# Optimization experiments

Measured on AMD Instinct MI355X. Metric: run time of the kernel, lower is better.

## Reference

```python
import jax, jax.numpy as jnp
from jax import lax
import numpy as np

HEADS = 4
BUCKET = 64
DEPTH = 4


def _conv(x, w, b):
    y = lax.conv_general_dilated(x, w, (1, 1), [(1, 1), (1, 1)],
                                 dimension_numbers=('NCHW', 'OIHW', 'NCHW'))
    return y + b[None, :, None, None]


def _convT(x, w, b):
    # torch ConvTranspose2d(k=4, s=2, p=1): flip kernel, swap io, lhs_dilation=2, pad k-1-p=2
    wk = jnp.flip(w, (2, 3)).transpose(1, 0, 2, 3)
    y = lax.conv_general_dilated(x, wk, (1, 1), [(2, 2), (2, 2)], lhs_dilation=(2, 2),
                                 dimension_numbers=('NCHW', 'OIHW', 'NCHW'))
    return y + b[None, :, None, None]


def _maxpool(x):
    return lax.reduce_window(x, -jnp.inf, lax.max, (1, 1, 2, 2), (1, 1, 2, 2), 'VALID')


def _ln(x, g, b):
    m = x.mean(-1, keepdims=True)
    v = ((x - m) ** 2).mean(-1, keepdims=True)
    return (x - m) / jnp.sqrt(v + 1e-5) * g + b


def _lsh_attention(x, Wqk, bqk, Wv, bv, Wo, bo, rot):
    # shared-QK LSH bucketed attention (single hash round), look-one-back chunks
    B, N, D = x.shape
    h, dh = HEADS, D // HEADS
    qk = (x @ Wqk + bqk).reshape(B, N, h, dh).transpose(0, 2, 1, 3)  # B h N dh
    v = (x @ Wv + bv).reshape(B, N, h, dh).transpose(0, 2, 1, 3)
    k = qk / (jnp.linalg.norm(qk, axis=-1, keepdims=True) + 1e-6)    # keys = normalized queries
    rotated = jnp.einsum('bhnd,hdr->bhnr', qk, rot)
    buckets = jnp.argmax(jnp.concatenate([rotated, -rotated], -1), -1)  # B h N
    ticker = jnp.arange(N)
    perm = jnp.argsort(buckets * N + ticker, axis=-1)  # stable sort by bucket
    inv_perm = jnp.argsort(perm, axis=-1)
    g = lambda t: jnp.take_along_axis(t, perm[..., None], axis=2)
    nc = N // BUCKET
    bq = g(qk).reshape(B, h, nc, BUCKET, dh)
    bk = g(k).reshape(B, h, nc, BUCKET, dh)
    bv_ = g(v).reshape(B, h, nc, BUCKET, dh)
    bk2 = jnp.concatenate([bk, jnp.roll(bk, 1, axis=2)], axis=3)   # look one chunk back
    bv2 = jnp.concatenate([bv_, jnp.roll(bv_, 1, axis=2)], axis=3)
    dots = jnp.einsum('bhcid,bhcjd->bhcij', bq, bk2) * (dh ** -0.5)
    spos = jnp.take_along_axis(jnp.broadcast_to(ticker, buckets.shape), perm, -1).reshape(B, h, nc, BUCKET)
    kpos = jnp.concatenate([spos, jnp.roll(spos, 1, axis=2)], axis=3)
    dots = jnp.where(spos[..., :, None] == kpos[..., None, :], -1e5, dots)  # mask self (q == k)
    attn = jax.nn.softmax(dots, -1)
    o = jnp.einsum('bhcij,bhcjd->bhcid', attn, bv2).reshape(B, h, N, dh)
    o = jnp.take_along_axis(o, inv_perm[..., None], axis=2)  # unsort
    return o.transpose(0, 2, 1, 3).reshape(B, N, D) @ Wo + bo


def _reformer(seq, ln1_g, ln1_b, Wqk, bqk, Wv, bv, Wo, bo, rot, ln2_g, ln2_b, Wff1, bff1, Wff2, bff2):
    for i in range(DEPTH):
        seq = seq + _lsh_attention(_ln(seq, ln1_g[i], ln1_b[i]), Wqk[i], bqk[i], Wv[i], bv[i], Wo[i], bo[i], rot[i])
        hdn = jax.nn.gelu(_ln(seq, ln2_g[i], ln2_b[i]) @ Wff1[i] + bff1[i])
        seq = seq + hdn @ Wff2[i] + bff2[i]
    return seq


def _forward(burst, conv1_w, conv1_b, conv2_w, conv2_b, conv3_w, conv3_b,
             ln1_g, ln1_b, Wqk, bqk, Wv, bv, Wo, bo, rot, ln2_g, ln2_b,
             Wff1, bff1, Wff2, bff2, up1_w, up1_b, dec1_w, dec1_b,
             up2_w, up2_b, dec2_w, dec2_b, out_w, out_b):
    B, T, C, H, W = burst.shape
    x = burst.reshape(B * T, C, H, W)
    e1 = jax.nn.relu(_conv(x, conv1_w, conv1_b))
    p1 = _maxpool(e1)
    e2 = jax.nn.relu(_conv(p1, conv2_w, conv2_b))
    p2 = _maxpool(e2)
    bm = jax.nn.relu(_conv(p2, conv3_w, conv3_b))
    D = bm.shape[1]
    Hq, Wq = H // 4, W // 4
    seq = bm.transpose(0, 2, 3, 1).reshape(B * T, Hq * Wq, D)
    seq = _reformer(seq, ln1_g, ln1_b, Wqk, bqk, Wv, bv, Wo, bo, rot, ln2_g, ln2_b, Wff1, bff1, Wff2, bff2)
    bm = seq.reshape(B * T, Hq, Wq, D).transpose(0, 3, 1, 2)
    d1 = _convT(bm, up1_w, up1_b)
    d1 = jax.nn.relu(_conv(jnp.concatenate([d1, e2], 1), dec1_w, dec1_b))
    d2 = _convT(d1, up2_w, up2_b)
    d2 = jax.nn.relu(_conv(jnp.concatenate([d2, e1], 1), dec2_w, dec2_b))
    sharp = jax.nn.sigmoid(_conv(d2, out_w, out_b))
    return sharp.reshape(B, T, C, H, W)[:, 0]


def setup_inputs() -> dict:
    key = jax.random.key(0)
    ks = jax.random.split(key, 20)
    s = 0.05
    n = lambda k, shape: jax.random.normal(k, shape, jnp.float32) * s
    inp = {}
    inp['burst'] = jax.random.uniform(ks[0], (1, 7, 3, 256, 256), jnp.float32)
    inp['conv1_w'] = n(ks[1], (64, 3, 3, 3)); inp['conv1_b'] = jnp.zeros((64,), jnp.float32)
    inp['conv2_w'] = n(ks[2], (128, 64, 3, 3)); inp['conv2_b'] = jnp.zeros((128,), jnp.float32)
    inp['conv3_w'] = n(ks[3], (256, 128, 3, 3)); inp['conv3_b'] = jnp.zeros((256,), jnp.float32)
    inp['ln1_g'] = jnp.ones((4, 256), jnp.float32); inp['ln1_b'] = jnp.zeros((4, 256), jnp.float32)
    inp['Wqk'] = n(ks[4], (4, 256, 256)); inp['bqk'] = jnp.zeros((4, 256), jnp.float32)
    inp['Wv'] = n(ks[5], (4, 256, 256)); inp['bv'] = jnp.zeros((4, 256), jnp.float32)
    inp['Wo'] = n(ks[6], (4, 256, 256)); inp['bo'] = jnp.zeros((4, 256), jnp.float32)
    inp['rot'] = jax.random.normal(ks[7], (4, 4, 64, 32), jnp.float32)  # depth, heads, d_head, n_buckets//2
    inp['ln2_g'] = jnp.ones((4, 256), jnp.float32); inp['ln2_b'] = jnp.zeros((4, 256), jnp.float32)
    inp['Wff1'] = n(ks[8], (4, 256, 1024)); inp['bff1'] = jnp.zeros((4, 1024), jnp.float32)
    inp['Wff2'] = n(ks[9], (4, 1024, 256)); inp['bff2'] = jnp.zeros((4, 256), jnp.float32)
    inp['up1_w'] = n(ks[10], (256, 128, 4, 4)); inp['up1_b'] = jnp.zeros((128,), jnp.float32)
    inp['dec1_w'] = n(ks[11], (128, 256, 3, 3)); inp['dec1_b'] = jnp.zeros((128,), jnp.float32)
    inp['up2_w'] = n(ks[12], (128, 64, 4, 4)); inp['up2_b'] = jnp.zeros((64,), jnp.float32)
    inp['dec2_w'] = n(ks[13], (64, 128, 3, 3)); inp['dec2_b'] = jnp.zeros((64,), jnp.float32)
    inp['out_w'] = n(ks[14], (3, 64, 3, 3)); inp['out_b'] = jnp.zeros((3,), jnp.float32)
    return inp


def reference(burst, conv1_w, conv1_b, conv2_w, conv2_b, conv3_w, conv3_b,
              ln1_g, ln1_b, Wqk, bqk, Wv, bv, Wo, bo, rot, ln2_g, ln2_b,
              Wff1, bff1, Wff2, bff2, up1_w, up1_b, dec1_w, dec1_b,
              up2_w, up2_b, dec2_w, dec2_b, out_w, out_b):
    return _forward(burst, conv1_w, conv1_b, conv2_w, conv2_b, conv3_w, conv3_b,
                    ln1_g, ln1_b, Wqk, bqk, Wv, bv, Wo, bo, rot, ln2_g, ln2_b,
                    Wff1, bff1, Wff2, bff2, up1_w, up1_b, dec1_w, dec1_b,
                    up2_w, up2_b, dec2_w, dec2_b, out_w, out_b)
```

## Files before the change

kernel.cpp:

```cpp
#include <hip/hip_runtime.h>
#include <hip/hip_bf16.h>
#include <math.h>

using short8  = __attribute__((ext_vector_type(8))) short;
using half8   = __attribute__((ext_vector_type(8))) _Float16;
using floatx4 = __attribute__((ext_vector_type(4))) float;

static __device__ __forceinline__ float gelu_f(float x) {
    float x3 = x * x * x;
    return 0.5f * x * (1.f + tanhf(0.7978845608028654f * (x + 0.044715f * x3)));
}

static __device__ __forceinline__ short f2h(float f) {
    _Float16 h = (_Float16)f;
    return __builtin_bit_cast(short, h);
}


template <int OCB>
__global__ __launch_bounds__(256) void conv3x3_kernel(
    const float* __restrict__ in1, int C1, const float* __restrict__ in2, int C2,
    const float* __restrict__ w, const float* __restrict__ bias,
    float* __restrict__ out, int H, int W, int OC, int act, int nhwc_out)
{
    int tx = threadIdx.x, ty = threadIdx.y;
    int x = blockIdx.x * 16 + tx, y = blockIdx.y * 16 + ty;
    int oc0 = blockIdx.z * OCB;
    int C = C1 + C2;
    float acc[OCB];
#pragma unroll
    for (int o = 0; o < OCB; ++o) acc[o] = 0.f;
    for (int ic = 0; ic < C; ++ic) {
        const float* src = (ic < C1) ? (in1 + (size_t)ic * H * W)
                                     : (in2 + (size_t)(ic - C1) * H * W);
        float v[9];
#pragma unroll
        for (int ky = 0; ky < 3; ++ky) {
            int iy = y + ky - 1;
            bool okY = (iy >= 0) && (iy < H);
#pragma unroll
            for (int kx = 0; kx < 3; ++kx) {
                int ix = x + kx - 1;
                bool ok = okY && (ix >= 0) && (ix < W);
                v[ky * 3 + kx] = ok ? src[(size_t)iy * W + ix] : 0.f;
            }
        }
        const float* wp = w + ((size_t)oc0 * C + ic) * 9;
#pragma unroll
        for (int o = 0; o < OCB; ++o) {
            const float* wo = wp + (size_t)o * C * 9;
            acc[o] += v[0]*wo[0] + v[1]*wo[1] + v[2]*wo[2]
                    + v[3]*wo[3] + v[4]*wo[4] + v[5]*wo[5]
                    + v[6]*wo[6] + v[7]*wo[7] + v[8]*wo[8];
        }
    }
#pragma unroll
    for (int o = 0; o < OCB; ++o) {
        int oc = oc0 + o;
        float r = acc[o] + bias[oc];
        if (act == 1) r = fmaxf(r, 0.f);
        else if (act == 2) r = 1.f / (1.f + expf(-r));
        if (nhwc_out) out[(size_t)(y * W + x) * OC + oc] = r;
        else          out[(size_t)oc * H * W + (size_t)y * W + x] = r;
    }
}

__global__ __launch_bounds__(256) void conv3x3_lds_kernel(
    const float* __restrict__ in, const float* __restrict__ w,
    const float* __restrict__ bias, float* __restrict__ out,
    int H, int W, int C, int OC, int nhwc_out)
{
    __shared__ float s[16 * 324];
    int tid = threadIdx.x;
    int tx = tid & 15, ty = tid >> 4;
    int x0 = blockIdx.x * 16, y0 = blockIdx.y * 16;
    int oc0 = blockIdx.z * 8;
    int HW = H * W;
    float acc[8];
#pragma unroll
    for (int o = 0; o < 8; ++o) acc[o] = 0.f;
    for (int ic0 = 0; ic0 < C; ic0 += 16) {
        __syncthreads();
        for (int idx = tid; idx < 16 * 324; idx += 256) {
            int ic = idx / 324;
            int r = idx - ic * 324;
            int yy = r / 18;
            int xx = r - yy * 18;
            int gy = y0 + yy - 1, gx = x0 + xx - 1;
            float v = 0.f;
            if (gy >= 0 && gy < H && gx >= 0 && gx < W)
                v = in[(size_t)(ic0 + ic) * HW + (size_t)gy * W + gx];
            s[idx] = v;
        }
        __syncthreads();
        for (int ic = 0; ic < 16; ++ic) {
            const float* sc = s + ic * 324;
            float v[9];
            v[0] = sc[(ty + 0) * 18 + tx + 0];
            v[1] = sc[(ty + 0) * 18 + tx + 1];
            v[2] = sc[(ty + 0) * 18 + tx + 2];
            v[3] = sc[(ty + 1) * 18 + tx + 0];
            v[4] = sc[(ty + 1) * 18 + tx + 1];
            v[5] = sc[(ty + 1) * 18 + tx + 2];
            v[6] = sc[(ty + 2) * 18 + tx + 0];
            v[7] = sc[(ty + 2) * 18 + tx + 1];
            v[8] = sc[(ty + 2) * 18 + tx + 2];
            const float* wp = w + ((size_t)oc0 * C + ic0 + ic) * 9;
#pragma unroll
            for (int o = 0; o < 8; ++o) {
                const float* wo = wp + (size_t)o * C * 9;
                acc[o] += v[0]*wo[0] + v[1]*wo[1] + v[2]*wo[2]
                        + v[3]*wo[3] + v[4]*wo[4] + v[5]*wo[5]
                        + v[6]*wo[6] + v[7]*wo[7] + v[8]*wo[8];
            }
        }
    }
    int x = x0 + tx, y = y0 + ty;
#pragma unroll
    for (int o = 0; o < 8; ++o) {
        int oc = oc0 + o;
        float r = fmaxf(acc[o] + bias[oc], 0.f);
        if (nhwc_out) out[(size_t)(y * W + x) * OC + oc] = r;
        else          out[(size_t)oc * HW + (size_t)y * W + x] = r;
    }
}

__global__ __launch_bounds__(256) void maxpool_kernel(
    const float* __restrict__ in, float* __restrict__ out, int C, int IH, int IW)
{
    int OH = IH >> 1, OW = IW >> 1;
    int idx = blockIdx.x * 256 + threadIdx.x;
    int total = C * OH * OW;
    if (idx >= total) return;
    int x = idx % OW; int t = idx / OW; int y = t % OH; int c = t / OH;
    const float* p = in + (size_t)c * IH * IW + (size_t)(2 * y) * IW + 2 * x;
    out[idx] = fmaxf(fmaxf(p[0], p[1]), fmaxf(p[IW], p[IW + 1]));
}

__global__ __launch_bounds__(256) void ln_kernel(
    const float* __restrict__ x, const float* __restrict__ g,
    const float* __restrict__ b, float* __restrict__ y, short* __restrict__ yh)
{
    int wave = threadIdx.x >> 6, lane = threadIdx.x & 63;
    int n = blockIdx.x * 4 + wave;
    const float* xr = x + (size_t)n * 256;
    float4 v = *(const float4*)(xr + lane * 4);
    float s = v.x + v.y + v.z + v.w;
#pragma unroll
    for (int m = 1; m < 64; m <<= 1) s += __shfl_xor(s, m);
    float mean = s * (1.f / 256.f);
    float cx = v.x - mean, cy = v.y - mean, cz = v.z - mean, cw = v.w - mean;
    float q = cx * cx + cy * cy + cz * cz + cw * cw;
#pragma unroll
    for (int m = 1; m < 64; m <<= 1) q += __shfl_xor(q, m);
    float rstd = rsqrtf(q * (1.f / 256.f) + 1e-5f);
    float4 gv = *(const float4*)(g + lane * 4);
    float4 bv = *(const float4*)(b + lane * 4);
    float4 o;
    o.x = cx * rstd * gv.x + bv.x;
    o.y = cy * rstd * gv.y + bv.y;
    o.z = cz * rstd * gv.z + bv.z;
    o.w = cw * rstd * gv.w + bv.w;
    *(float4*)(y + (size_t)n * 256 + lane * 4) = o;
    short* yp = yh + (size_t)n * 256 + lane * 4;
    yp[0] = f2h(o.x); yp[1] = f2h(o.y); yp[2] = f2h(o.z); yp[3] = f2h(o.w);
}

static __device__ __forceinline__ void gemm_core(
    const float* __restrict__ A, const float* __restrict__ W,
    const float* __restrict__ bias, float* __restrict__ Cp,
    int N, int K, int act, int resid, int m0, int n0)
{
    __shared__ float As[16][68];
    __shared__ float Ws[16][68];
    int tid = threadIdx.x;
    int tx = tid & 15, ty = tid >> 4;
    int lm = tid & 63, lk = (tid >> 6) * 4;
    int lwk = tid >> 4, lwn = (tid & 15) * 4;
    const float* Ap = A + (size_t)(m0 + lm) * K + lk;
    const float* Wp = W + (size_t)lwk * N + n0 + lwn;
    float4 av = *(const float4*)Ap;
    float4 wv = *(const float4*)Wp;
    float acc[4][4];
#pragma unroll
    for (int i = 0; i < 4; ++i)
#pragma unroll
        for (int j = 0; j < 4; ++j) acc[i][j] = 0.f;
    for (int k0 = 0; k0 < K; k0 += 16) {
        As[lk + 0][lm] = av.x; As[lk + 1][lm] = av.y;
        As[lk + 2][lm] = av.z; As[lk + 3][lm] = av.w;
        *(float4*)(&Ws[lwk][lwn]) = wv;
        __syncthreads();
        if (k0 + 16 < K) {
            av = *(const float4*)(Ap + k0 + 16);
            wv = *(const float4*)(Wp + (size_t)(k0 + 16) * N);
        }
#pragma unroll
        for (int kk = 0; kk < 16; ++kk) {
            float4 a4 = *(const float4*)(&As[kk][ty * 4]);
            float4 w4 = *(const float4*)(&Ws[kk][tx * 4]);
            acc[0][0] += a4.x * w4.x; acc[0][1] += a4.x * w4.y; acc[0][2] += a4.x * w4.z; acc[0][3] += a4.x * w4.w;
            acc[1][0] += a4.y * w4.x; acc[1][1] += a4.y * w4.y; acc[1][2] += a4.y * w4.z; acc[1][3] += a4.y * w4.w;
            acc[2][0] += a4.z * w4.x; acc[2][1] += a4.z * w4.y; acc[2][2] += a4.z * w4.z; acc[2][3] += a4.z * w4.w;
            acc[3][0] += a4.w * w4.x; acc[3][1] += a4.w * w4.y; acc[3][2] += a4.w * w4.z; acc[3][3] += a4.w * w4.w;
        }
        __syncthreads();
    }
#pragma unroll
    for (int i = 0; i < 4; ++i) {
        int cm = m0 + ty * 4 + i;
#pragma unroll
        for (int j = 0; j < 4; ++j) {
            int cn = n0 + tx * 4 + j;
            float v = acc[i][j] + bias[cn];
            if (act == 1) v = gelu_f(v);
            float* cp = Cp + (size_t)cm * N + cn;
            if (resid) v += *cp;
            *cp = v;
        }
    }
}

__global__ __launch_bounds__(256) void gemm_kernel(
    const float* __restrict__ A, const float* __restrict__ W,
    const float* __restrict__ bias, float* __restrict__ C,
    int M, int N, int K, int act, int resid)
{
    gemm_core(A, W, bias, C, N, K, act, resid, blockIdx.y * 64, blockIdx.x * 64);
}

__global__ __launch_bounds__(256) void gemm_qkv_kernel(
    const float* __restrict__ A,
    const float* __restrict__ W1, const float* __restrict__ b1, float* __restrict__ C1,
    const float* __restrict__ W2, const float* __restrict__ b2, float* __restrict__ C2,
    int K)
{
    int side = blockIdx.x >> 2;
    const float* W = side ? W2 : W1;
    const float* b = side ? b2 : b1;
    float* C = side ? C2 : C1;
    gemm_core(A, W, b, C, 256, K, 0, 0, blockIdx.y * 64, (blockIdx.x & 3) * 64);
}

__global__ __launch_bounds__(256) void knorm_kernel(
    const float* __restrict__ qk, float* __restrict__ knrm)
{
    int t = blockIdx.x * 256 + threadIdx.x;
    int h = t >> 12, n = t & 4095;
    const float* q = qk + (size_t)n * 256 + h * 64;
    float s = 0.f;
#pragma unroll
    for (int d = 0; d < 64; d += 4) {
        float4 v = *(const float4*)(q + d);
        s += v.x * v.x + v.y * v.y + v.z * v.z + v.w * v.w;
    }
    knrm[t] = 1.f / (sqrtf(s) + 1e-6f);
}

__global__ __launch_bounds__(256) void bucket_kernel(
    const float* __restrict__ qk, const float* __restrict__ rot,
    int* __restrict__ buckets)
{
    int t = blockIdx.x * 256 + threadIdx.x;
    int h = t >> 12, n = t & 4095;
    const float* q = qk + (size_t)n * 256 + h * 64;
    const float* R = rot + (size_t)h * 2048;
    float acc[32];
#pragma unroll
    for (int r = 0; r < 32; ++r) acc[r] = 0.f;
    for (int d = 0; d < 64; ++d) {
        float qd = q[d];
        const float* Rd = R + d * 32;
#pragma unroll
        for (int r = 0; r < 32; ++r) acc[r] += qd * Rd[r];
    }
    float bvv = acc[0]; int best = 0;
#pragma unroll
    for (int j = 1; j < 64; ++j) {
        float val = (j < 32) ? acc[j] : -acc[j - 32];
        if (val > bvv) { bvv = val; best = j; }
    }
    buckets[t] = best;
}

__global__ __launch_bounds__(256) void lsh_sort_kernel(
    const int* __restrict__ buckets, int* __restrict__ perm)
{
    int h = blockIdx.x;
    const int* bk = buckets + h * 4096;
    __shared__ unsigned long long mask[64][64];
    __shared__ int counts[64];
    __shared__ int offsets[64];
    __shared__ int wpre[64][64];
    int tid = threadIdx.x, wave = tid >> 6, lane = tid & 63;
    for (int w = wave * 16; w < wave * 16 + 16; ++w) {
        int bl = bk[w * 64 + lane];
        for (int b = 0; b < 64; ++b) {
            unsigned long long m = __ballot(bl == b);
            if (lane == b) mask[b][w] = m;
        }
    }
    __syncthreads();
    if (tid < 64) {
        int c = 0;
        for (int w = 0; w < 64; ++w) c += __popcll(mask[tid][w]);
        counts[tid] = c;
    }
    __syncthreads();
    if (tid == 0) {
        int a = 0;
        for (int b = 0; b < 64; ++b) { offsets[b] = a; a += counts[b]; }
    }
    __syncthreads();
    for (int b = wave * 16; b < wave * 16 + 16; ++b) {
        int c = __popcll(mask[b][lane]);
        int incl = c;
#pragma unroll
        for (int off = 1; off < 64; off <<= 1) {
            int nb = __shfl_up(incl, off);
            if (lane >= off) incl += nb;
        }
        wpre[b][lane] = incl - c + offsets[b];
    }
    __syncthreads();
    for (int i = tid; i < 4096; i += 256) {
        int b = bk[i]; int w = i >> 6; int l = i & 63;
        unsigned long long below = mask[b][w] & ((1ull << l) - 1ull);
        int pos = wpre[b][w] + __popcll(below);
        perm[h * 4096 + pos] = i;
    }
}

__global__ __launch_bounds__(256) void attn_kernel(
    const float* __restrict__ qk, const float* __restrict__ vv,
    const float* __restrict__ knrm, const int* __restrict__ perm,
    float* __restrict__ o, short* __restrict__ oh)
{
    __shared__ float ks[128 * 64];
    __shared__ float dotsT[128 * 64];
    int c = blockIdx.x, h = blockIdx.y;
    int tid = threadIdx.x;
    const int* pm = perm + h * 4096;
    int cm = (c + 63) & 63;
    {
        int jr = tid >> 1, hf = tid & 1;
        int sk = (jr < 64) ? (c * 64 + jr) : (cm * 64 + (jr - 64));
        int nk = pm[sk];
        float sc = knrm[h * 4096 + nk];
        const float* src = qk + (size_t)nk * 256 + h * 64 + hf * 32;
        float* dst = ks + jr * 64 + hf * 32;
#pragma unroll
        for (int d = 0; d < 32; d += 4) {
            float4 v = *(const float4*)(src + d);
            v.x *= sc; v.y *= sc; v.z *= sc; v.w *= sc;
            *(float4*)(dst + d) = v;
        }
    }
    __syncthreads();
    int r = tid & 63, jg = tid >> 6;
    int nq = pm[c * 64 + r];
    {
        float qreg[64];
        const float* src = qk + (size_t)nq * 256 + h * 64;
#pragma unroll
        for (int d = 0; d < 64; d += 4) {
            float4 v = *(const float4*)(src + d);
            qreg[d] = v.x; qreg[d + 1] = v.y; qreg[d + 2] = v.z; qreg[d + 3] = v.w;
        }
        for (int j = jg * 32; j < jg * 32 + 32; ++j) {
            const float* kr = ks + j * 64;
            float dot = 0.f;
#pragma unroll
            for (int d = 0; d < 64; ++d) dot += qreg[d] * kr[d];
            int sk = (j < 64) ? (c * 64 + j) : (cm * 64 + (j - 64));
            int nk = pm[sk];
            dot = (nk == nq) ? -1e5f : dot * 0.125f;
            dotsT[j * 64 + r] = dot;
        }
    }
    __syncthreads();
    {
        int jr = tid >> 1, hf = tid & 1;
        int sk = (jr < 64) ? (c * 64 + jr) : (cm * 64 + (jr - 64));
        int nk = pm[sk];
        const float* src = vv + (size_t)nk * 256 + h * 64 + hf * 32;
        float* dst = ks + jr * 64 + hf * 32;
#pragma unroll
        for (int d = 0; d < 32; d += 4)
            *(float4*)(dst + d) = *(const float4*)(src + d);
    }
    if (tid < 64) {
        int rr = tid;
        float mx = -1e30f;
        for (int j = 0; j < 128; ++j) mx = fmaxf(mx, dotsT[j * 64 + rr]);
        float s = 0.f;
        for (int j = 0; j < 128; ++j) {
            float e = expf(dotsT[j * 64 + rr] - mx);
            dotsT[j * 64 + rr] = e; s += e;
        }
        float inv = 1.f / s;
        for (int j = 0; j < 128; ++j) dotsT[j * 64 + rr] *= inv;
    }
    __syncthreads();
    int dg = jg;
    float acc[16];
#pragma unroll
    for (int d = 0; d < 16; ++d) acc[d] = 0.f;
    for (int j = 0; j < 128; ++j) {
        float a = dotsT[j * 64 + r];
        const float* vr = ks + j * 64 + dg * 16;
#pragma unroll
        for (int d = 0; d < 16; ++d) acc[d] += a * vr[d];
    }
    size_t ob = (size_t)nq * 256 + h * 64 + dg * 16;
    float* dst = o + ob;
    short* dsth = oh + ob;
#pragma unroll
    for (int d = 0; d < 16; d += 4) {
        float4 v = { acc[d], acc[d + 1], acc[d + 2], acc[d + 3] };
        *(float4*)(dst + d) = v;
        dsth[d] = f2h(v.x); dsth[d+1] = f2h(v.y);
        dsth[d+2] = f2h(v.z); dsth[d+3] = f2h(v.w);
    }
}


__global__ void pack_gemm_kernel(const float* __restrict__ W, short* __restrict__ Bp,
                                 int N, int total)
{
    int t = blockIdx.x * 256 + threadIdx.x;
    if (t >= total) return;
    int lane = t & 63, fi = t >> 6;
    int NT = N >> 4;
    int nt = fi % NT, kt = fi / NT;
    int n = nt * 16 + (lane & 15);
    int k0 = kt * 32 + (lane >> 4) * 8;
    short8 v;
#pragma unroll
    for (int j = 0; j < 8; ++j) v[j] = f2h(W[(size_t)(k0 + j) * N + n]);
    ((short8*)Bp)[t] = v;
}

__global__ void pack_conv_kernel(const float* __restrict__ w, short* __restrict__ Bp,
                                 int C, int OC, int NT, int total)
{
    int t = blockIdx.x * 256 + threadIdx.x;
    if (t >= total) return;
    int lane = t & 63, fi = t >> 6;
    int nt = fi % NT, kt = fi / NT;
    int cpt = C >> 5;
    int tap = kt / cpt, ct = kt % cpt;
    int c = ct * 32 + (lane >> 4) * 8;
    int oc = nt * 16 + (lane & 15);
    short8 v;
#pragma unroll
    for (int j = 0; j < 8; ++j) {
        float f = (oc < OC) ? w[((size_t)oc * C + c + j) * 9 + tap] : 0.f;
        v[j] = f2h(f);
    }
    ((short8*)Bp)[t] = v;
}

__global__ void pack_convt_kernel(const float* __restrict__ w, short* __restrict__ Bp,
                                  int IC, int OC, int total)
{
    int t = blockIdx.x * 256 + threadIdx.x;
    if (t >= total) return;
    int lane = t & 63, fi = t >> 6;
    int NT = OC >> 4, cpt = IC >> 5, KT4 = 4 * cpt;
    int nt = fi % NT, r = fi / NT;
    int kt = r % KT4, pz = r / KT4;
    int py = pz >> 1, px = pz & 1;
    int t4 = kt / cpt, ct = kt % cpt;
    int ty = t4 >> 1, tx = t4 & 1;
    int ky = py ? (2 * ty) : (1 + 2 * ty);
    int kx = px ? (2 * tx) : (1 + 2 * tx);
    int ic = ct * 32 + (lane >> 4) * 8;
    int oc = nt * 16 + (lane & 15);
    short8 v;
#pragma unroll
    for (int j = 0; j < 8; ++j)
        v[j] = f2h(w[(((size_t)(ic + j) * OC + oc) * 4 + ky) * 4 + kx]);
    ((short8*)Bp)[t] = v;
}

__global__ __launch_bounds__(256) void gemm_mfma_kernel(
    const short* __restrict__ A, const short* __restrict__ Bp,
    const float* __restrict__ bias, float* __restrict__ Cf, short* __restrict__ Cb,
    int M, int N, int K, int act, int resid)
{
    int tid = threadIdx.x, wave = tid >> 6, lane = tid & 63;
    int quad = lane >> 4, l16 = lane & 15;
    int m0 = blockIdx.y * 64 + wave * 16;
    int NT = N >> 4;
    int nt0 = blockIdx.x * 4;
    const half8* arow = (const half8*)(A + (size_t)(m0 + l16) * K + quad * 8);
    const half8* bp = (const half8*)Bp;
    floatx4 acc0 = {0,0,0,0}, acc1 = {0,0,0,0}, acc2 = {0,0,0,0}, acc3 = {0,0,0,0};
    int KT = K >> 5;
    for (int kt = 0; kt < KT; ++kt) {
        half8 a = arow[kt * 4];
        size_t bi = ((size_t)kt * NT + nt0) * 64 + lane;
        acc0 = __builtin_amdgcn_mfma_f32_16x16x32_f16(a, bp[bi      ], acc0, 0, 0, 0);
        acc1 = __builtin_amdgcn_mfma_f32_16x16x32_f16(a, bp[bi +  64], acc1, 0, 0, 0);
        acc2 = __builtin_amdgcn_mfma_f32_16x16x32_f16(a, bp[bi + 128], acc2, 0, 0, 0);
        acc3 = __builtin_amdgcn_mfma_f32_16x16x32_f16(a, bp[bi + 192], acc3, 0, 0, 0);
    }
    floatx4 accs[4] = {acc0, acc1, acc2, acc3};
#pragma unroll
    for (int s = 0; s < 4; ++s) {
        int n = (nt0 + s) * 16 + l16;
        float bs = bias[n];
#pragma unroll
        for (int r = 0; r < 4; ++r) {
            int m = m0 + quad * 4 + r;
            float v = accs[s][r] + bs;
            if (act == 1) v = gelu_f(v);
            size_t o = (size_t)m * N + n;
            if (resid) v += Cf[o];
            if (Cb) Cb[o] = f2h(v);
            else    Cf[o] = v;
        }
    }
}

__global__ __launch_bounds__(256) void conv_mfma_kernel(
    const short* __restrict__ in1, int C1, const short* __restrict__ in2, int C2,
    const short* __restrict__ Bp, const float* __restrict__ bias,
    float* __restrict__ outf, short* __restrict__ outb, int H, int W, int OC)
{
    int tid = threadIdx.x, wave = tid >> 6, lane = tid & 63;
    int quad = lane >> 4, l16 = lane & 15;
    int x0 = blockIdx.x * 64, y = blockIdx.y, nt0 = blockIdx.z * 4;
    int C = C1 + C2, cpt = C >> 5, NT = OC >> 4;
    const half8* bp = (const half8*)Bp;
    floatx4 acc0 = {0,0,0,0}, acc1 = {0,0,0,0}, acc2 = {0,0,0,0}, acc3 = {0,0,0,0};
    int xm = x0 + wave * 16 + l16;
    for (int ky = 0; ky < 3; ++ky) {
        int yy = y + ky - 1;
        bool rok = (yy >= 0) && (yy < H);
        for (int kx = 0; kx < 3; ++kx) {
            int xx = xm + kx - 1;
            bool ok = rok && (xx >= 0) && (xx < W);
            int pos = yy * W + xx;
            int ktb = (ky * 3 + kx) * cpt;
            for (int ct = 0; ct < cpt; ++ct) {
                int cc = ct * 32 + quad * 8;
                half8 a = {};
                if (ok) {
                    const short* src = (cc < C1) ? (in1 + (size_t)pos * C1 + cc)
                                                 : (in2 + (size_t)pos * C2 + (cc - C1));
                    a = *(const half8*)src;
                }
                size_t bi = ((size_t)(ktb + ct) * NT + nt0) * 64 + lane;
                acc0 = __builtin_amdgcn_mfma_f32_16x16x32_f16(a, bp[bi      ], acc0, 0, 0, 0);
                acc1 = __builtin_amdgcn_mfma_f32_16x16x32_f16(a, bp[bi +  64], acc1, 0, 0, 0);
                acc2 = __builtin_amdgcn_mfma_f32_16x16x32_f16(a, bp[bi + 128], acc2, 0, 0, 0);
                acc3 = __builtin_amdgcn_mfma_f32_16x16x32_f16(a, bp[bi + 192], acc3, 0, 0, 0);
            }
        }
    }
    floatx4 accs[4] = {acc0, acc1, acc2, acc3};
#pragma unroll
    for (int s = 0; s < 4; ++s) {
        int n = (nt0 + s) * 16 + l16;
        float bs = bias[n];
#pragma unroll
        for (int r = 0; r < 4; ++r) {
            int m = wave * 16 + quad * 4 + r;
            int x = x0 + m;
            float v = fmaxf(accs[s][r] + bs, 0.f);
            size_t o = ((size_t)y * W + x) * OC + n;
            if (outb) outb[o] = f2h(v);
            else      outf[o] = v;
        }
    }
}

__global__ __launch_bounds__(256) void convt_mfma_kernel(
    const short* __restrict__ in, int IC, const short* __restrict__ Bp,
    const float* __restrict__ bias, short* __restrict__ outb, int IH, int IW, int OC)
{
    int tid = threadIdx.x, wave = tid >> 6, lane = tid & 63;
    int quad = lane >> 4, l16 = lane & 15;
    int pz = blockIdx.z & 3, nt0 = (blockIdx.z >> 2) * 4;
    int py = pz >> 1, px = pz & 1;
    int a0 = blockIdx.y, b0 = blockIdx.x * 64;
    int cpt = IC >> 5, NT = OC >> 4, KT4 = 4 * cpt;
    const half8* bp = (const half8*)Bp;
    floatx4 acc0 = {0,0,0,0}, acc1 = {0,0,0,0}, acc2 = {0,0,0,0}, acc3 = {0,0,0,0};
    int bm = b0 + wave * 16 + l16;
    for (int ty = 0; ty < 2; ++ty) {
        int iy = a0 + (py ? (1 - ty) : (-ty));
        bool rok = (iy >= 0) && (iy < IH);
        for (int tx = 0; tx < 2; ++tx) {
            int ix = bm + (px ? (1 - tx) : (-tx));
            bool ok = rok && (ix >= 0) && (ix < IW);
            int pos = iy * IW + ix;
            int ktb = (ty * 2 + tx) * cpt;
            for (int ct = 0; ct < cpt; ++ct) {
                int cc = ct * 32 + quad * 8;
                half8 a = {};
                if (ok) a = *(const half8*)(in + (size_t)pos * IC + cc);
                size_t bi = ((size_t)(pz * KT4 + ktb + ct) * NT + nt0) * 64 + lane;
                acc0 = __builtin_amdgcn_mfma_f32_16x16x32_f16(a, bp[bi      ], acc0, 0, 0, 0);
                acc1 = __builtin_amdgcn_mfma_f32_16x16x32_f16(a, bp[bi +  64], acc1, 0, 0, 0);
                acc2 = __builtin_amdgcn_mfma_f32_16x16x32_f16(a, bp[bi + 128], acc2, 0, 0, 0);
                acc3 = __builtin_amdgcn_mfma_f32_16x16x32_f16(a, bp[bi + 192], acc3, 0, 0, 0);
            }
        }
    }
    floatx4 accs[4] = {acc0, acc1, acc2, acc3};
    int OW = IW * 2;
    int oy = 2 * a0 + py;
#pragma unroll
    for (int s = 0; s < 4; ++s) {
        int n = (nt0 + s) * 16 + l16;
        float bs = bias[n];
#pragma unroll
        for (int r = 0; r < 4; ++r) {
            int m = wave * 16 + quad * 4 + r;
            int ox = 2 * (b0 + m) + px;
            float v = accs[s][r] + bs;
            outb[((size_t)oy * OW + ox) * OC + n] = f2h(v);
        }
    }
}

__global__ __launch_bounds__(256) void convout_mfma_kernel(
    const short* __restrict__ in, const short* __restrict__ Bp,
    const float* __restrict__ bias, float* __restrict__ out, int H, int W)
{
    int tid = threadIdx.x, wave = tid >> 6, lane = tid & 63;
    int quad = lane >> 4, l16 = lane & 15;
    int x0 = blockIdx.x * 64, y = blockIdx.y;
    const int C = 64, cpt = 2;
    const half8* bp = (const half8*)Bp;
    floatx4 acc = {0,0,0,0};
    int xm = x0 + wave * 16 + l16;
    for (int ky = 0; ky < 3; ++ky) {
        int yy = y + ky - 1;
        bool rok = (yy >= 0) && (yy < H);
        for (int kx = 0; kx < 3; ++kx) {
            int xx = xm + kx - 1;
            bool ok = rok && (xx >= 0) && (xx < W);
            int pos = yy * W + xx;
            int ktb = (ky * 3 + kx) * cpt;
#pragma unroll
            for (int ct = 0; ct < cpt; ++ct) {
                int cc = ct * 32 + quad * 8;
                half8 a = {};
                if (ok) a = *(const half8*)(in + (size_t)pos * C + cc);
                acc = __builtin_amdgcn_mfma_f32_16x16x32_f16(
                          a, bp[(size_t)(ktb + ct) * 64 + lane], acc, 0, 0, 0);
            }
        }
    }
    int oc = l16;
    if (oc < 3) {
        float bs = bias[oc];
#pragma unroll
        for (int r = 0; r < 4; ++r) {
            int m = wave * 16 + quad * 4 + r;
            int x = x0 + m;
            float v = acc[r] + bs;
            v = 1.f / (1.f + expf(-v));
            out[(size_t)oc * H * W + (size_t)y * W + x] = v;
        }
    }
}

__global__ __launch_bounds__(256) void nchw2nhwc_h_kernel(
    const float* __restrict__ in, short* __restrict__ out, int C, int HW)
{
    __shared__ float t[32][33];
    int c0 = blockIdx.y * 32, p0 = blockIdx.x * 32;
    int tid = threadIdx.x;
#pragma unroll
    for (int it = 0; it < 4; ++it) {
        int i = tid + it * 256;
        int lc = i >> 5, lp = i & 31;
        t[lc][lp] = in[(size_t)(c0 + lc) * HW + p0 + lp];
    }
    __syncthreads();
#pragma unroll
    for (int it = 0; it < 4; ++it) {
        int i = tid + it * 256;
        int lp = i >> 5, lc = i & 31;
        out[(size_t)(p0 + lp) * C + c0 + lc] = f2h(t[lc][lp]);
    }
}

__global__ __launch_bounds__(256) void f2h_kernel(
    const float* __restrict__ in, short* __restrict__ out, int n)
{
    int i = blockIdx.x * 256 + threadIdx.x;
    if (i < n) out[i] = f2h(in[i]);
}

extern "C" void kernel_launch(void* const* d_in, const int* in_sizes, int n_in,
                              void* d_out, int out_size, void* d_ws, size_t ws_size,
                              hipStream_t stream)
{
    const float* burst   = (const float*)d_in[0];
    const float* conv1_w = (const float*)d_in[1];  const float* conv1_b = (const float*)d_in[2];
    const float* conv2_w = (const float*)d_in[3];  const float* conv2_b = (const float*)d_in[4];
    const float* conv3_w = (const float*)d_in[5];  const float* conv3_b = (const float*)d_in[6];
    const float* ln1_g   = (const float*)d_in[7];  const float* ln1_b   = (const float*)d_in[8];
    const float* Wqk     = (const float*)d_in[9];  const float* bqk     = (const float*)d_in[10];
    const float* Wv      = (const float*)d_in[11]; const float* bvv     = (const float*)d_in[12];
    const float* Wo      = (const float*)d_in[13]; const float* bo      = (const float*)d_in[14];
    const float* rot     = (const float*)d_in[15];
    const float* ln2_g   = (const float*)d_in[16]; const float* ln2_b   = (const float*)d_in[17];
    const float* Wff1    = (const float*)d_in[18]; const float* bff1    = (const float*)d_in[19];
    const float* Wff2    = (const float*)d_in[20]; const float* bff2    = (const float*)d_in[21];
    const float* up1_w   = (const float*)d_in[22]; const float* up1_b   = (const float*)d_in[23];
    const float* dec1_w  = (const float*)d_in[24]; const float* dec1_b  = (const float*)d_in[25];
    const float* up2_w   = (const float*)d_in[26]; const float* up2_b   = (const float*)d_in[27];
    const float* dec2_w  = (const float*)d_in[28]; const float* dec2_b  = (const float*)d_in[29];
    const float* out_w   = (const float*)d_in[30]; const float* out_b   = (const float*)d_in[31];

    float* ws = (float*)d_ws;
    float* e1   = ws + 0;
    float* e2   = ws + 4194304;
    float* p1   = ws + 6291456;
    float* p2   = ws + 7340032;
    float* seq  = ws + 7864320;
    float* xn   = ws + 8912896;
    float* qkb  = ws + 9961472;
    float* vvb  = ws + 11010048;
    float* oob  = ws + 12058624;
    float* hdn  = ws + 13107200;
    float* knb  = ws + 17301504;
    int* buckets = (int*)(ws + 17317888);
    int* perm    = (int*)(ws + 17334272);
    short* xnh  = (short*)p1;
    short* seqh = (short*)(ws + 6815744);
    short* ooh  = (short*)p2;
    short* hdnh = (short*)hdn;
    short* e1h  = (short*)(ws + 15204352);
    short* e2h  = (short*)vvb;
    short* d1   = (short*)xn;
    short* d1c  = (short*)qkb;
    short* d2   = (short*)hdn;
    short* d2c  = (short*)e2;
    short* pk    = (short*)(ws + 17350656);
    short* ppo   = pk + 65536;
    short* ppf1  = pk + 131072;
    short* ppf2  = pk + 393216;
    short* pdec1 = pk + 655360;
    short* pdec2 = pk + 950272;
    short* pout  = pk + 1024000;
    short* pup1  = pk + 1033216;
    short* pup2  = pk + 1557504;

    dim3 b16(16, 16);

    pack_gemm_kernel<<<32, 256, 0, stream>>>(Wo  + 3 * 65536,  ppo,  256, 8192);
    pack_gemm_kernel<<<128, 256, 0, stream>>>(Wff1 + 3 * 262144, ppf1, 1024, 32768);
    pack_gemm_kernel<<<128, 256, 0, stream>>>(Wff2 + 3 * 262144, ppf2, 256, 32768);
    pack_conv_kernel<<<144, 256, 0, stream>>>(dec1_w, pdec1, 256, 128, 8, 36864);
    pack_conv_kernel<<<36, 256, 0, stream>>>(dec2_w, pdec2, 128, 64, 4, 9216);
    pack_conv_kernel<<<5, 256, 0, stream>>>(out_w,  pout,  64, 3, 1, 1152);
    pack_convt_kernel<<<256, 256, 0, stream>>>(up1_w, pup1, 256, 128, 65536);
    pack_convt_kernel<<<64, 256, 0, stream>>>(up2_w, pup2, 128, 64, 16384);

    conv3x3_kernel<8><<<dim3(16, 16, 8), b16, 0, stream>>>(
        burst, 3, nullptr, 0, conv1_w, conv1_b, e1, 256, 256, 64, 1, 0);
    maxpool_kernel<<<4096, 256, 0, stream>>>(e1, p1, 64, 256, 256);
    conv3x3_lds_kernel<<<dim3(8, 8, 16), 256, 0, stream>>>(
        p1, conv2_w, conv2_b, e2, 128, 128, 64, 128, 0);
    maxpool_kernel<<<2048, 256, 0, stream>>>(e2, p2, 128, 128, 128);
    conv3x3_lds_kernel<<<dim3(4, 4, 32), 256, 0, stream>>>(
        p2, conv3_w, conv3_b, seq, 64, 64, 128, 256, 1);

    for (int i = 0; i < 3; ++i) {
        ln_kernel<<<1024, 256, 0, stream>>>(seq, ln1_g + i * 256, ln1_b + i * 256, xn, xnh);
        gemm_qkv_kernel<<<dim3(8, 64), 256, 0, stream>>>(
            xn, Wqk + i * 65536, bqk + i * 256, qkb,
            Wv + i * 65536, bvv + i * 256, vvb, 256);
        knorm_kernel<<<64, 256, 0, stream>>>(qkb, knb);
        bucket_kernel<<<64, 256, 0, stream>>>(qkb, rot + i * 8192, buckets);
        lsh_sort_kernel<<<4, 256, 0, stream>>>(buckets, perm);
        attn_kernel<<<dim3(64, 4), 256, 0, stream>>>(qkb, vvb, knb, perm, oob, ooh);
        gemm_kernel<<<dim3(4, 64), 256, 0, stream>>>(oob, Wo + i * 65536, bo + i * 256,
                                                     seq, 4096, 256, 256, 0, 1);
        ln_kernel<<<1024, 256, 0, stream>>>(seq, ln2_g + i * 256, ln2_b + i * 256, xn, xnh);
        gemm_kernel<<<dim3(16, 64), 256, 0, stream>>>(xn, Wff1 + i * 262144, bff1 + i * 1024,
                                                      hdn, 4096, 1024, 256, 1, 0);
        gemm_kernel<<<dim3(4, 64), 256, 0, stream>>>(hdn, Wff2 + i * 262144, bff2 + i * 256,
                                                     seq, 4096, 256, 1024, 0, 1);
    }

    {
        const int i = 3;
        ln_kernel<<<1024, 256, 0, stream>>>(seq, ln1_g + i * 256, ln1_b + i * 256, xn, xnh);
        gemm_qkv_kernel<<<dim3(8, 64), 256, 0, stream>>>(
            xn, Wqk + i * 65536, bqk + i * 256, qkb,
            Wv + i * 65536, bvv + i * 256, vvb, 256);
        knorm_kernel<<<64, 256, 0, stream>>>(qkb, knb);
        bucket_kernel<<<64, 256, 0, stream>>>(qkb, rot + i * 8192, buckets);
        lsh_sort_kernel<<<4, 256, 0, stream>>>(buckets, perm);
        attn_kernel<<<dim3(64, 4), 256, 0, stream>>>(qkb, vvb, knb, perm, oob, ooh);
        gemm_mfma_kernel<<<dim3(4, 64), 256, 0, stream>>>(
            ooh, ppo, bo + i * 256, seq, nullptr, 4096, 256, 256, 0, 1);
        ln_kernel<<<1024, 256, 0, stream>>>(seq, ln2_g + i * 256, ln2_b + i * 256, xn, xnh);
        gemm_mfma_kernel<<<dim3(16, 64), 256, 0, stream>>>(
            xnh, ppf1, bff1 + i * 1024, nullptr, hdnh, 4096, 1024, 256, 1, 0);
        gemm_mfma_kernel<<<dim3(4, 64), 256, 0, stream>>>(
            hdnh, ppf2, bff2 + i * 256, seq, nullptr, 4096, 256, 1024, 0, 1);
    }

    nchw2nhwc_h_kernel<<<dim3(2048, 2), 256, 0, stream>>>(e1, e1h, 64, 65536);
    nchw2nhwc_h_kernel<<<dim3(512, 4), 256, 0, stream>>>(e2, e2h, 128, 16384);
    f2h_kernel<<<4096, 256, 0, stream>>>(seq, seqh, 1048576);

    convt_mfma_kernel<<<dim3(1, 64, 8), 256, 0, stream>>>(
        seqh, 256, pup1, up1_b, d1, 64, 64, 128);
    conv_mfma_kernel<<<dim3(2, 128, 2), 256, 0, stream>>>(
        d1, 128, e2h, 128, pdec1, dec1_b, nullptr, d1c, 128, 128, 128);
    convt_mfma_kernel<<<dim3(2, 128, 4), 256, 0, stream>>>(
        d1c, 128, pup2, up2_b, d2, 128, 128, 64);
    conv_mfma_kernel<<<dim3(4, 256, 1), 256, 0, stream>>>(
        d2, 64, e1h, 64, pdec2, dec2_b, nullptr, d2c, 256, 256, 64);
    convout_mfma_kernel<<<dim3(4, 256), 256, 0, stream>>>(
        d2c, pout, out_b, (float*)d_out, 256, 256);
}
```

Before: 1.431 ms.

## Switch encoder convs to NHWC with transposing maxpool and double-buffered GEMM LDS

The maxpools now write NHWC output through an LDS transpose. Conv2 and conv3 use a new NHWC direct-convolution kernel that reads float4 vectors along the channel dimension, with weights pre-packed into [oc][tap][ic] order. This replaces the LDS-tiled NCHW conv, which staged halo tiles and synchronised for every group of 16 input channels. The FP32 GEMM core gets double-buffered shared memory, which removes the second barrier per k-tile. The new conv reads inputs from global memory without LDS reuse and relies on caches, which may cost more memory traffic.

After: 1.474 ms. 1.03x slower.

```diff
diff --git a/kernel.cpp b/kernel.cpp
--- a/kernel.cpp
+++ b/kernel.cpp
@@ -19,20 +19,19 @@
 
 template <int OCB>
 __global__ __launch_bounds__(256) void conv3x3_kernel(
-    const float* __restrict__ in1, int C1, const float* __restrict__ in2, int C2,
+    const float* __restrict__ in1, int C1,
     const float* __restrict__ w, const float* __restrict__ bias,
-    float* __restrict__ out, int H, int W, int OC, int act, int nhwc_out)
+    float* __restrict__ out, int H, int W, int OC)
 {
     int tx = threadIdx.x, ty = threadIdx.y;
     int x = blockIdx.x * 16 + tx, y = blockIdx.y * 16 + ty;
     int oc0 = blockIdx.z * OCB;
-    int C = C1 + C2;
+    int C = C1;
     float acc[OCB];
 #pragma unroll
     for (int o = 0; o < OCB; ++o) acc[o] = 0.f;
     for (int ic = 0; ic < C; ++ic) {
-        const float* src = (ic < C1) ? (in1 + (size_t)ic * H * W)
-                                     : (in2 + (size_t)(ic - C1) * H * W);
+        const float* src = in1 + (size_t)ic * H * W;
         float v[9];
 #pragma unroll
         for (int ky = 0; ky < 3; ++ky) {
@@ -57,84 +56,81 @@
 #pragma unroll
     for (int o = 0; o < OCB; ++o) {
         int oc = oc0 + o;
-        float r = acc[o] + bias[oc];
-        if (act == 1) r = fmaxf(r, 0.f);
-        else if (act == 2) r = 1.f / (1.f + expf(-r));
-        if (nhwc_out) out[(size_t)(y * W + x) * OC + oc] = r;
-        else          out[(size_t)oc * H * W + (size_t)y * W + x] = r;
-    }
-}
-
-__global__ __launch_bounds__(256) void conv3x3_lds_kernel(
-    const float* __restrict__ in, const float* __restrict__ w,
+        out[(size_t)oc * H * W + (size_t)y * W + x] = fmaxf(acc[o] + bias[oc], 0.f);
+    }
+}
+
+__global__ void pack_convw_f32_kernel(const float* __restrict__ w,
+                                      float* __restrict__ pw, int C, int OC)
+{
+    int i = blockIdx.x * 256 + threadIdx.x;
+    if (i >= OC * C * 9) return;
+    int ic = i % C; int r = i / C; int tap = r % 9; int oc = r / 9;
+    pw[i] = w[((size_t)oc * C + ic) * 9 + tap];
+}
+
+__global__ __launch_bounds__(256) void maxpool_t_kernel(
+    const float* __restrict__ in, float* __restrict__ out, int C, int IH, int IW)
+{
+    __shared__ float t[32][33];
+    int OH = IH >> 1, OW = IW >> 1;
+    int c0 = blockIdx.y * 32, p0 = blockIdx.x * 32;
+    int tid = threadIdx.x;
+#pragma unroll
+    for (int it = 0; it < 4; ++it) {
+        int i = tid + it * 256;
+        int lc = i >> 5, lp = i & 31;
+        int p = p0 + lp; int x = p % OW; int y = p / OW;
+        const float* q = in + (size_t)(c0 + lc) * IH * IW + (size_t)(2 * y) * IW + 2 * x;
+        t[lc][lp] = fmaxf(fmaxf(q[0], q[1]), fmaxf(q[IW], q[IW + 1]));
+    }
+    __syncthreads();
+#pragma unroll
+    for (int it = 0; it < 4; ++it) {
+        int i = tid + it * 256;
+        int lp = i >> 5, lc = i & 31;
+        out[(size_t)(p0 + lp) * C + c0 + lc] = t[lc][lp];
+    }
+}
+
+template <int OCB>
+__global__ __launch_bounds__(256) void conv3x3_nhwc_kernel(
+    const float* __restrict__ in, const float* __restrict__ wp,
     const float* __restrict__ bias, float* __restrict__ out,
     int H, int W, int C, int OC, int nhwc_out)
 {
-    __shared__ float s[16 * 324];
-    int tid = threadIdx.x;
-    int tx = tid & 15, ty = tid >> 4;
-    int x0 = blockIdx.x * 16, y0 = blockIdx.y * 16;
-    int oc0 = blockIdx.z * 8;
-    int HW = H * W;
-    float acc[8];
-#pragma unroll
-    for (int o = 0; o < 8; ++o) acc[o] = 0.f;
-    for (int ic0 = 0; ic0 < C; ic0 += 16) {
-        __syncthreads();
-        for (int idx = tid; idx < 16 * 324; idx += 256) {
-            int ic = idx / 324;
-            int r = idx - ic * 324;
-            int yy = r / 18;
-            int xx = r - yy * 18;
-            int gy = y0 + yy - 1, gx = x0 + xx - 1;
-            float v = 0.f;
-            if (gy >= 0 && gy < H && gx >= 0 && gx < W)
-                v = in[(size_t)(ic0 + ic) * HW + (size_t)gy * W + gx];
-            s[idx] = v;
-        }
-        __syncthreads();
-        for (int ic = 0; ic < 16; ++ic) {
-            const float* sc = s + ic * 324;
-            float v[9];
-            v[0] = sc[(ty + 0) * 18 + tx + 0];
-            v[1] = sc[(ty + 0) * 18 + tx + 1];
-            v[2] = sc[(ty + 0) * 18 + tx + 2];
-            v[3] = sc[(ty + 1) * 18 + tx + 0];
-            v[4] = sc[(ty + 1) * 18 + tx + 1];
-            v[5] = sc[(ty + 1) * 18 + tx + 2];
-            v[6] = sc[(ty + 2) * 18 + tx + 0];
-            v[7] = sc[(ty + 2) * 18 + tx + 1];
-            v[8] = sc[(ty + 2) * 18 + tx + 2];
-            const float* wp = w + ((size_t)oc0 * C + ic0 + ic) * 9;
-#pragma unroll
-            for (int o = 0; o < 8; ++o) {
-                const float* wo = wp + (size_t)o * C * 9;
-                acc[o] += v[0]*wo[0] + v[1]*wo[1] + v[2]*wo[2]
-                        + v[3]*wo[3] + v[4]*wo[4] + v[5]*wo[5]
-                        + v[6]*wo[6] + v[7]*wo[7] + v[8]*wo[8];
+    int tid = threadIdx.x, tx = tid & 15, ty = tid >> 4;
+    int x = blockIdx.x * 16 + tx, y = blockIdx.y * 16 + ty;
+    int oc0 = blockIdx.z * OCB;
+    float acc[OCB];
+#pragma unroll
+    for (int o = 0; o < OCB; ++o) acc[o] = 0.f;
+    for (int ky = 0; ky < 3; ++ky) {
+        int iy = y + ky - 1;
+        bool okY = (iy >= 0) && (iy < H);
+        for (int kx = 0; kx < 3; ++kx) {
+            int ix = x + kx - 1;
+            bool ok = okY && (ix >= 0) && (ix < W);
+            const float* pin = in + ((size_t)iy * W + ix) * C;
+            int tap = ky * 3 + kx;
+            for (int ic = 0; ic < C; ic += 4) {
+                float4 v = {0.f, 0.f, 0.f, 0.f};
+                if (ok) v = *(const float4*)(pin + ic);
+#pragma unroll
+                for (int o = 0; o < OCB; ++o) {
+                    const float* wo = wp + ((size_t)(oc0 + o) * 9 + tap) * C + ic;
+                    acc[o] += v.x * wo[0] + v.y * wo[1] + v.z * wo[2] + v.w * wo[3];
+                }
             }
         }
     }
-    int x = x0 + tx, y = y0 + ty;
-#pragma unroll
-    for (int o = 0; o < 8; ++o) {
+#pragma unroll
+    for (int o = 0; o < OCB; ++o) {
         int oc = oc0 + o;
         float r = fmaxf(acc[o] + bias[oc], 0.f);
         if (nhwc_out) out[(size_t)(y * W + x) * OC + oc] = r;
-        else          out[(size_t)oc * HW + (size_t)y * W + x] = r;
-    }
-}
-
-__global__ __launch_bounds__(256) void maxpool_kernel(
-    const float* __restrict__ in, float* __restrict__ out, int C, int IH, int IW)
-{
-    int OH = IH >> 1, OW = IW >> 1;
-    int idx = blockIdx.x * 256 + threadIdx.x;
-    int total = C * OH * OW;
-    if (idx >= total) return;
-    int x = idx % OW; int t = idx / OW; int y = t % OH; int c = t / OH;
-    const float* p = in + (size_t)c * IH * IW + (size_t)(2 * y) * IW + 2 * x;
-    out[idx] = fmaxf(fmaxf(p[0], p[1]), fmaxf(p[IW], p[IW + 1]));
+        else          out[(size_t)oc * H * W + (size_t)y * W + x] = r;
+    }
 }
 
 __global__ __launch_bounds__(256) void ln_kernel(
@@ -171,8 +167,8 @@
     const float* __restrict__ bias, float* __restrict__ Cp,
     int N, int K, int act, int resid, int m0, int n0)
 {
-    __shared__ float As[16][68];
-    __shared__ float Ws[16][68];
+    __shared__ float As[2][16][68];
+    __shared__ float Ws[2][16][68];
     int tid = threadIdx.x;
     int tx = tid & 15, ty = tid >> 4;
     int lm = tid & 63, lk = (tid >> 6) * 4;
@@ -186,25 +182,26 @@
     for (int i = 0; i < 4; ++i)
 #pragma unroll
         for (int j = 0; j < 4; ++j) acc[i][j] = 0.f;
-    for (int k0 = 0; k0 < K; k0 += 16) {
-        As[lk + 0][lm] = av.x; As[lk + 1][lm] = av.y;
-        As[lk + 2][lm] = av.z; As[lk + 3][lm] = av.w;
-        *(float4*)(&Ws[lwk][lwn]) = wv;
+    int KT = K >> 4;
+    for (int kt = 0; kt < KT; ++kt) {
+        int b = kt & 1;
+        As[b][lk + 0][lm] = av.x; As[b][lk + 1][lm] = av.y;
+        As[b][lk + 2][lm] = av.z; As[b][lk + 3][lm] = av.w;
+        *(float4*)(&Ws[b][lwk][lwn]) = wv;
         __syncthreads();
-        if (k0 + 16 < K) {
-            av = *(const float4*)(Ap + k0 + 16);
-            wv = *(const float4*)(Wp + (size_t)(k0 + 16) * N);
+        if (kt + 1 < KT) {
+            av = *(const float4*)(Ap + (kt + 1) * 16);
+            wv = *(const float4*)(Wp + (size_t)((kt + 1) * 16) * N);
         }
 #pragma unroll
         for (int kk = 0; kk < 16; ++kk) {
-            float4 a4 = *(const float4*)(&As[kk][ty * 4]);
-            float4 w4 = *(const float4*)(&Ws[kk][tx * 4]);
+            float4 a4 = *(const float4*)(&As[b][kk][ty * 4]);
+            float4 w4 = *(const float4*)(&Ws[b][kk][tx * 4]);
             acc[0][0] += a4.x * w4.x; acc[0][1] += a4.x * w4.y; acc[0][2] += a4.x * w4.z; acc[0][3] += a4.x * w4.w;
             acc[1][0] += a4.y * w4.x; acc[1][1] += a4.y * w4.y; acc[1][2] += a4.y * w4.z; acc[1][3] += a4.y * w4.w;
             acc[2][0] += a4.z * w4.x; acc[2][1] += a4.z * w4.y; acc[2][2] += a4.z * w4.z; acc[2][3] += a4.z * w4.w;
             acc[3][0] += a4.w * w4.x; acc[3][1] += a4.w * w4.y; acc[3][2] += a4.w * w4.z; acc[3][3] += a4.w * w4.w;
         }
-        __syncthreads();
     }
 #pragma unroll
     for (int i = 0; i < 4; ++i) {
@@ -723,8 +720,6 @@
     float* ws = (float*)d_ws;
     float* e1   = ws + 0;
     float* e2   = ws + 4194304;
-    float* p1   = ws + 6291456;
-    float* p2   = ws + 7340032;
     float* seq  = ws + 7864320;
     float* xn   = ws + 8912896;
     float* qkb  = ws + 9961472;
@@ -734,9 +729,13 @@
     float* knb  = ws + 17301504;
     int* buckets = (int*)(ws + 17317888);
     int* perm    = (int*)(ws + 17334272);
-    short* xnh  = (short*)p1;
+    float* p1t  = hdn;
+    float* p2t  = hdn + 1048576;
+    float* pwc2 = hdn + 1572864;
+    float* pwc3 = hdn + 1646592;
+    short* xnh  = (short*)(ws + 6291456);
     short* seqh = (short*)(ws + 6815744);
-    short* ooh  = (short*)p2;
+    short* ooh  = (short*)(ws + 7340032);
     short* hdnh = (short*)hdn;
     short* e1h  = (short*)(ws + 15204352);
     short* e2h  = (short*)vvb;
@@ -756,6 +755,8 @@
 
     dim3 b16(16, 16);
 
+    pack_convw_f32_kernel<<<288, 256, 0, stream>>>(conv2_w, pwc2, 64, 128);
+    pack_convw_f32_kernel<<<1152, 256, 0, stream>>>(conv3_w, pwc3, 128, 256);
     pack_gemm_kernel<<<32, 256, 0, stream>>>(Wo  + 3 * 65536,  ppo,  256, 8192);
     pack_gemm_kernel<<<128, 256, 0, stream>>>(Wff1 + 3 * 262144, ppf1, 1024, 32768);
     pack_gemm_kernel<<<128, 256, 0, stream>>>(Wff2 + 3 * 262144, ppf2, 256, 32768);
@@ -766,13 +767,13 @@
     pack_convt_kernel<<<64, 256, 0, stream>>>(up2_w, pup2, 128, 64, 16384);
 
     conv3x3_kernel<8><<<dim3(16, 16, 8), b16, 0, stream>>>(
-        burst, 3, nullptr, 0, conv1_w, conv1_b, e1, 256, 256, 64, 1, 0);
-    maxpool_kernel<<<4096, 256, 0, stream>>>(e1, p1, 64, 256, 256);
-    conv3x3_lds_kernel<<<dim3(8, 8, 16), 256, 0, stream>>>(
-        p1, conv2_w, conv2_b, e2, 128, 128, 64, 128, 0);
-    maxpool_kernel<<<2048, 256, 0, stream>>>(e2, p2, 128, 128, 128);
-    conv3x3_lds_kernel<<<dim3(4, 4, 32), 256, 0, stream>>>(
-        p2, conv3_w, conv3_b, seq, 64, 64, 128, 256, 1);
+        burst, 3, conv1_w, conv1_b, e1, 256, 256, 64);
+    maxpool_t_kernel<<<dim3(512, 2), 256, 0, stream>>>(e1, p1t, 64, 256, 256);
+    conv3x3_nhwc_kernel<16><<<dim3(8, 8, 8), 256, 0, stream>>>(
+        p1t, pwc2, conv2_b, e2, 128, 128, 64, 128, 0);
+    maxpool_t_kernel<<<dim3(128, 4), 256, 0, stream>>>(e2, p2t, 128, 128, 128);
+    conv3x3_nhwc_kernel<8><<<dim3(4, 4, 32), 256, 0, stream>>>(
+        p2t, pwc3, conv3_b, seq, 64, 64, 128, 256, 1);
 
     for (int i = 0; i < 3; ++i) {
         ln_kernel<<<1024, 256, 0, stream>>>(seq, ln1_g + i * 256, ln1_b + i * 256, xn, xnh);
```
